# Kernel tuning notes

Hardware: AMD Instinct MI355X
Metric: run time of the kernel (lower is better)

The kernel has to match this reference:

```python
import jax, jax.numpy as jnp
import numpy as np

DIM = 512
HEADS = 8
DIM_HEAD = 64
DIM_INNER = HEADS * DIM_HEAD  # 512
EPS = 1e-12


def setup_inputs() -> dict:
    key = jax.random.key(0)
    ks = jax.random.split(key, 5)
    B, X, Y, N = 8, 32, 32, 1024
    fmap = jax.random.normal(ks[0], (B, DIM, X, Y), dtype=jnp.float32)
    context = jax.random.normal(ks[1], (B, N, DIM), dtype=jnp.float32)
    gamma_fmap = jnp.ones((DIM, 1, 1), dtype=jnp.float32)
    gamma_ctx = jnp.ones((DIM,), dtype=jnp.float32)
    Wq = jax.random.normal(ks[2], (DIM_INNER, DIM), dtype=jnp.float32) * 0.02
    Wkv = jax.random.normal(ks[3], (2 * DIM_INNER, DIM), dtype=jnp.float32) * 0.02
    Wout = jax.random.normal(ks[4], (DIM, DIM_INNER), dtype=jnp.float32) * 0.02
    return {"fmap": fmap, "context": context, "gamma_fmap": gamma_fmap,
            "gamma_ctx": gamma_ctx, "Wq": Wq, "Wkv": Wkv, "Wout": Wout}


def _channel_rmsnorm(x, gamma):
    # F.normalize(x, dim=1) * sqrt(dim) * gamma ; x: [b, c, x, y]
    norm = jnp.sqrt(jnp.sum(x * x, axis=1, keepdims=True))
    normed = x / jnp.maximum(norm, EPS)
    return normed * (DIM ** 0.5) * gamma


def _rmsnorm(x, gamma):
    # F.normalize(x, dim=-1) * sqrt(dim) * gamma ; x: [b, n, d]
    norm = jnp.sqrt(jnp.sum(x * x, axis=-1, keepdims=True))
    normed = x / jnp.maximum(norm, EPS)
    return normed * (DIM ** 0.5) * gamma


def reference(fmap, context, gamma_fmap, gamma_ctx, Wq, Wkv, Wout):
    B, _, X, Y = fmap.shape
    N = context.shape[1]
    H, D = HEADS, DIM_HEAD
    scale = D ** -0.5

    fm = _channel_rmsnorm(fmap, gamma_fmap)          # [b, c, x, y]
    ctx = _rmsnorm(context, gamma_ctx)               # [b, n, c]

    # 1x1 conv == channel matmul
    q = jnp.einsum('bcxy,ec->bexy', fm, Wq)          # [b, h*d, x, y]
    kv = jnp.einsum('bnc,ec->bne', ctx, Wkv)         # [b, n, 2*h*d]
    k, v = jnp.split(kv, 2, axis=-1)

    # q: b (h d) x y -> (b h) (x y) d
    q = q.reshape(B, H, D, X * Y).transpose(0, 1, 3, 2).reshape(B * H, X * Y, D)
    # k, v: b n (h d) -> (b h) n d
    k = k.reshape(B, N, H, D).transpose(0, 2, 1, 3).reshape(B * H, N, D)
    v = v.reshape(B, N, H, D).transpose(0, 2, 1, 3).reshape(B * H, N, D)

    # Euclidean cdist: sqrt(||q||^2 + ||k||^2 - 2 q.k)
    q2 = jnp.sum(q * q, axis=-1)                     # [bh, i]
    k2 = jnp.sum(k * k, axis=-1)                     # [bh, j]
    qk = jnp.einsum('bid,bjd->bij', q, k)            # [bh, i, j]
    dist = jnp.sqrt(jnp.maximum(q2[:, :, None] + k2[:, None, :] - 2.0 * qk, 0.0))
    sim = -dist * scale
    attn = jax.nn.softmax(sim, axis=-1)

    out = jnp.einsum('bij,bjd->bid', attn, v)        # [bh, xy, d]
    # (b h) (x y) d -> b (h d) x y
    out = out.reshape(B, H, X * Y, D).transpose(0, 1, 3, 2).reshape(B, H * D, X, Y)
    return jnp.einsum('bexy,de->bdxy', out, Wout)    # [b, dim, x, y]
```

## Files before the change

### kernel.cpp

```cpp
#include <hip/hip_runtime.h>
#include <math.h>

#define BATCH 8
#define CDIM 512
#define XY 1024
#define NCTX 1024
#define HEADS 8
#define DHEAD 64
#define EINNER 512
#define E2 1024

#define SQRT_DIM 22.627416997969522f

typedef short bf16x8 __attribute__((ext_vector_type(8)));
typedef float f32x4 __attribute__((ext_vector_type(4)));
typedef unsigned short ushort4v __attribute__((ext_vector_type(4)));

__device__ __forceinline__ unsigned short f2bf(float x) {
    unsigned int u = __builtin_bit_cast(unsigned int, x);
    return (unsigned short)((u + 0x7fffu + ((u >> 16) & 1u)) >> 16);
}
__device__ __forceinline__ float bf2f(unsigned short h) {
    unsigned int u = ((unsigned int)h) << 16;
    return __builtin_bit_cast(float, u);
}

__global__ __launch_bounds__(256) void k_fmap_scale(const float* __restrict__ fmap,
                                                    float* __restrict__ fscale) {
    int t = blockIdx.x * 256 + threadIdx.x;
    int b = t >> 10;
    const float* p = fmap + (size_t)b * CDIM * XY + (t & 1023);
    float ss = 0.f;
#pragma unroll 8
    for (int c = 0; c < CDIM; ++c) {
        float v = p[(size_t)c * XY];
        ss = fmaf(v, v, ss);
    }
    fscale[t] = SQRT_DIM / fmaxf(sqrtf(ss), 1e-12f);
}

__global__ __launch_bounds__(256) void k_ctx_scale(const float* __restrict__ ctx,
                                                   float* __restrict__ cscale) {
    int row = blockIdx.x * 4 + (threadIdx.x >> 6);
    int lane = threadIdx.x & 63;
    const float* p = ctx + (size_t)row * CDIM;
    float ss = 0.f;
#pragma unroll
    for (int k = 0; k < CDIM / 64; ++k) {
        float v = p[lane + 64 * k];
        ss = fmaf(v, v, ss);
    }
#pragma unroll
    for (int off = 32; off; off >>= 1) ss += __shfl_down(ss, off, 64);
    if (lane == 0) cscale[row] = SQRT_DIM / fmaxf(sqrtf(ss), 1e-12f);
}

template <bool SCALE_B>
__global__ __launch_bounds__(256) void k_gemm_nn(const float* __restrict__ A,
                                                 const float* __restrict__ Bm,
                                                 float* __restrict__ Cm,
                                                 const float* __restrict__ colscale,
                                                 const float* __restrict__ rowgamma,
                                                 int M, int N, int K) {
    const int b = blockIdx.z;
    const int n0 = blockIdx.x * 64, m0 = blockIdx.y * 64;
    const float* Bb = Bm + (size_t)b * K * N;
    float* Cb = Cm + (size_t)b * M * N;
    __shared__ float As[16][68];
    __shared__ float Bs[16][68];
    const int t = threadIdx.x;
    const int tr = t >> 4, tc = t & 15;
    const int la_k = t & 15, la_m = t >> 4;
    const int lb_n = t & 63, lb_k = t >> 6;
    float acc[4][4] = {};

    float cs = 1.f;
    if constexpr (SCALE_B) cs = colscale[(size_t)b * N + n0 + lb_n];

    for (int k0 = 0; k0 < K; k0 += 16) {
        __syncthreads();
#pragma unroll
        for (int i = 0; i < 4; ++i) {
            int m = la_m + 16 * i;
            As[la_k][m] = A[(size_t)(m0 + m) * K + k0 + la_k];
        }
#pragma unroll
        for (int i = 0; i < 4; ++i) {
            int kk = lb_k + 4 * i;
            float v = Bb[(size_t)(k0 + kk) * N + n0 + lb_n];
            if constexpr (SCALE_B) v *= cs * rowgamma[k0 + kk];
            Bs[kk][lb_n] = v;
        }
        __syncthreads();
#pragma unroll
        for (int kk = 0; kk < 16; ++kk) {
            const float4 a4 = *(const float4*)(&As[kk][tr * 4]);
            const float4 b4 = *(const float4*)(&Bs[kk][tc * 4]);
            const float ar[4] = {a4.x, a4.y, a4.z, a4.w};
            const float bc[4] = {b4.x, b4.y, b4.z, b4.w};
#pragma unroll
            for (int rr = 0; rr < 4; ++rr)
#pragma unroll
                for (int cc = 0; cc < 4; ++cc)
                    acc[rr][cc] = fmaf(ar[rr], bc[cc], acc[rr][cc]);
        }
    }
#pragma unroll
    for (int rr = 0; rr < 4; ++rr) {
        float4 v = {acc[rr][0], acc[rr][1], acc[rr][2], acc[rr][3]};
        *(float4*)(&Cb[(size_t)(m0 + tr * 4 + rr) * N + n0 + tc * 4]) = v;
    }
}

__global__ __launch_bounds__(256) void k_gemm_kv(const float* __restrict__ Am,
                                                 const float* __restrict__ Bmat,
                                                 const float* __restrict__ rowscale,
                                                 const float* __restrict__ kgamma,
                                                 unsigned short* __restrict__ khi,
                                                 unsigned short* __restrict__ klo,
                                                 unsigned short* __restrict__ vthi,
                                                 unsigned short* __restrict__ vtlo,
                                                 float* __restrict__ k2g) {
    const int b = blockIdx.z;
    const int M = NCTX, K = CDIM;
    const int n0 = blockIdx.x * 64, m0 = blockIdx.y * 64;
    const float* Ab = Am + (size_t)b * M * K;
    __shared__ float As[16][68];
    __shared__ float Bs[16][68];
    const int t = threadIdx.x;
    const int tr = t >> 4, tc = t & 15;
    const int la_k = t & 15, la_m = t >> 4;
    float acc[4][4] = {};

    float rs[4];
#pragma unroll
    for (int i = 0; i < 4; ++i)
        rs[i] = rowscale[(size_t)b * M + m0 + la_m + 16 * i];

    for (int k0 = 0; k0 < K; k0 += 16) {
        __syncthreads();
#pragma unroll
        for (int i = 0; i < 4; ++i) {
            int m = la_m + 16 * i;
            float v = Ab[(size_t)(m0 + m) * K + k0 + la_k];
            v *= rs[i] * kgamma[k0 + la_k];
            As[la_k][m] = v;
        }
#pragma unroll
        for (int i = 0; i < 4; ++i) {
            int n = la_m + 16 * i;
            Bs[la_k][n] = Bmat[(size_t)(n0 + n) * K + k0 + la_k];
        }
        __syncthreads();
#pragma unroll
        for (int kk = 0; kk < 16; ++kk) {
            const float4 a4 = *(const float4*)(&As[kk][tr * 4]);
            const float4 b4 = *(const float4*)(&Bs[kk][tc * 4]);
            const float ar[4] = {a4.x, a4.y, a4.z, a4.w};
            const float bc[4] = {b4.x, b4.y, b4.z, b4.w};
#pragma unroll
            for (int rr = 0; rr < 4; ++rr)
#pragma unroll
                for (int cc = 0; cc < 4; ++cc)
                    acc[rr][cc] = fmaf(ar[rr], bc[cc], acc[rr][cc]);
        }
    }

    const int hh = (n0 >> 6) & 7;
    const int bh_i = b * 8 + hh;
    if (n0 < EINNER) {
#pragma unroll
        for (int rr = 0; rr < 4; ++rr) {
            const int n = m0 + tr * 4 + rr;
            ushort4v h4, l4;
#pragma unroll
            for (int cc = 0; cc < 4; ++cc) {
                unsigned short h = f2bf(acc[rr][cc]);
                h4[cc] = h;
                l4[cc] = f2bf(acc[rr][cc] - bf2f(h));
            }
            *(ushort4v*)(khi + ((size_t)bh_i * NCTX + n) * 64 + tc * 4) = h4;
            *(ushort4v*)(klo + ((size_t)bh_i * NCTX + n) * 64 + tc * 4) = l4;
        }
#pragma unroll
        for (int rr = 0; rr < 4; ++rr) {
            float s = 0.f;
#pragma unroll
            for (int cc = 0; cc < 4; ++cc) s = fmaf(acc[rr][cc], acc[rr][cc], s);
            s += __shfl_xor(s, 1, 64);
            s += __shfl_xor(s, 2, 64);
            s += __shfl_xor(s, 4, 64);
            s += __shfl_xor(s, 8, 64);
            if (tc == 0) k2g[(size_t)bh_i * NCTX + m0 + tr * 4 + rr] = s;
        }
    } else {
#pragma unroll
        for (int cc = 0; cc < 4; ++cc) {
            const int d = tc * 4 + cc;
            ushort4v h4, l4;
#pragma unroll
            for (int rr = 0; rr < 4; ++rr) {
                unsigned short h = f2bf(acc[rr][cc]);
                h4[rr] = h;
                l4[rr] = f2bf(acc[rr][cc] - bf2f(h));
            }
            *(ushort4v*)(vthi + ((size_t)bh_i * 64 + d) * NCTX + m0 + tr * 4) = h4;
            *(ushort4v*)(vtlo + ((size_t)bh_i * 64 + d) * NCTX + m0 + tr * 4) = l4;
        }
    }
}

__global__ __launch_bounds__(256) void k_attn_mfma(
    const float* __restrict__ qbuf, const unsigned short* __restrict__ khi,
    const unsigned short* __restrict__ klo, const unsigned short* __restrict__ vthi,
    const unsigned short* __restrict__ vtlo, const float* __restrict__ k2g,
    float* __restrict__ ao) {
    const int bh = blockIdx.y;
    const int i0 = blockIdx.x * 32;
    const int t = threadIdx.x;
    const int w = t >> 6;
    const int rg = w >> 1;
    const int jh = w & 1;
    const int lane = t & 63;
    const int c = lane & 15, g = lane >> 4;

    __shared__ __align__(16) char pool[18432];
    unsigned short* psth = (unsigned short*)(pool + w * 4608);
    unsigned short* pstl = psth + 16 * 72;
    __shared__ float q2s[32];
    __shared__ float msh[4][16];
    __shared__ float lsh[4][16];

    const float* qb = qbuf + (size_t)bh * 64 * XY;
    const int qrow = i0 + 16 * rg + c;
    float qv[16];
#pragma unroll
    for (int kk = 0; kk < 2; ++kk)
#pragma unroll
        for (int i = 0; i < 8; ++i)
            qv[kk * 8 + i] = qb[(size_t)(32 * kk + 8 * g + i) * XY + qrow];

    float s2 = 0.f;
#pragma unroll
    for (int i = 0; i < 16; ++i) s2 = fmaf(qv[i], qv[i], s2);
    s2 += __shfl_xor(s2, 16, 64);
    s2 += __shfl_xor(s2, 32, 64);
    if (g == 0) q2s[16 * rg + c] = s2;
    __syncthreads();
    float q2r[4];
#pragma unroll
    for (int r = 0; r < 4; ++r) q2r[r] = q2s[16 * rg + 4 * g + r];

    bf16x8 qh[2], ql[2];
#pragma unroll
    for (int kk = 0; kk < 2; ++kk)
#pragma unroll
        for (int i = 0; i < 8; ++i) {
            float x = qv[kk * 8 + i];
            unsigned short h = f2bf(x);
            qh[kk][i] = (short)h;
            ql[kk][i] = (short)f2bf(x - bf2f(h));
        }

    const unsigned short* khb = khi + (size_t)bh * NCTX * 64;
    const unsigned short* klb = klo + (size_t)bh * NCTX * 64;
    const unsigned short* vhb = vthi + (size_t)bh * 64 * NCTX;
    const unsigned short* vlb = vtlo + (size_t)bh * 64 * NCTX;
    const float* k2b = k2g + (size_t)bh * NCTX;

    f32x4 acc_o[4] = {{0.f, 0.f, 0.f, 0.f}, {0.f, 0.f, 0.f, 0.f},
                      {0.f, 0.f, 0.f, 0.f}, {0.f, 0.f, 0.f, 0.f}};
    float m_run[4], l_run[4];
#pragma unroll
    for (int r = 0; r < 4; ++r) { m_run[r] = -1e30f; l_run[r] = 0.f; }

    const int jbeg = jh * 512, jend = jbeg + 512;
    for (int j0 = jbeg; j0 < jend; j0 += 64) {
        float p[4][4];
#pragma unroll
        for (int cc = 0; cc < 4; ++cc) {
            const unsigned short* kr_h = khb + (size_t)(j0 + 16 * cc + c) * 64 + 8 * g;
            const unsigned short* kr_l = klb + (size_t)(j0 + 16 * cc + c) * 64 + 8 * g;
            f32x4 acc = {0.f, 0.f, 0.f, 0.f};
#pragma unroll
            for (int kk = 0; kk < 2; ++kk) {
                bf16x8 kh_ = *(const bf16x8*)(kr_h + 32 * kk);
                bf16x8 kl_ = *(const bf16x8*)(kr_l + 32 * kk);
                acc = __builtin_amdgcn_mfma_f32_16x16x32_bf16(qh[kk], kh_, acc, 0, 0, 0);
                acc = __builtin_amdgcn_mfma_f32_16x16x32_bf16(qh[kk], kl_, acc, 0, 0, 0);
                acc = __builtin_amdgcn_mfma_f32_16x16x32_bf16(ql[kk], kh_, acc, 0, 0, 0);
            }
            float k2v = k2b[j0 + 16 * cc + c];
#pragma unroll
            for (int r = 0; r < 4; ++r) {
                float d2 = q2r[r] + k2v - 2.f * acc[r];
                p[cc][r] = -0.125f * sqrtf(fmaxf(d2, 0.f));
            }
        }
        float alpha[4];
#pragma unroll
        for (int r = 0; r < 4; ++r) {
            float mt = fmaxf(fmaxf(p[0][r], p[1][r]), fmaxf(p[2][r], p[3][r]));
            mt = fmaxf(mt, __shfl_xor(mt, 1, 64));
            mt = fmaxf(mt, __shfl_xor(mt, 2, 64));
            mt = fmaxf(mt, __shfl_xor(mt, 4, 64));
            mt = fmaxf(mt, __shfl_xor(mt, 8, 64));
            float mn = fmaxf(m_run[r], mt);
            alpha[r] = __expf(m_run[r] - mn);
            m_run[r] = mn;
            float sum = 0.f;
#pragma unroll
            for (int cc = 0; cc < 4; ++cc) {
                float e = __expf(p[cc][r] - mn);
                p[cc][r] = e;
                sum += e;
            }
            sum += __shfl_xor(sum, 1, 64);
            sum += __shfl_xor(sum, 2, 64);
            sum += __shfl_xor(sum, 4, 64);
            sum += __shfl_xor(sum, 8, 64);
            l_run[r] = l_run[r] * alpha[r] + sum;
        }
#pragma unroll
        for (int dt = 0; dt < 4; ++dt)
#pragma unroll
            for (int r = 0; r < 4; ++r) acc_o[dt][r] *= alpha[r];

#pragma unroll
        for (int cc = 0; cc < 4; ++cc)
#pragma unroll
            for (int r = 0; r < 4; ++r) {
                float x = p[cc][r];
                unsigned short h = f2bf(x);
                psth[(4 * g + r) * 72 + 16 * cc + c] = h;
                pstl[(4 * g + r) * 72 + 16 * cc + c] = f2bf(x - bf2f(h));
            }
        asm volatile("s_waitcnt lgkmcnt(0)" ::: "memory");
        bf16x8 ph[2], pl[2];
#pragma unroll
        for (int kk = 0; kk < 2; ++kk) {
            ph[kk] = *(const bf16x8*)(psth + c * 72 + 32 * kk + 8 * g);
            pl[kk] = *(const bf16x8*)(pstl + c * 72 + 32 * kk + 8 * g);
        }
#pragma unroll
        for (int dt = 0; dt < 4; ++dt) {
            const unsigned short* vr_h = vhb + (size_t)(16 * dt + c) * NCTX + j0 + 8 * g;
            const unsigned short* vr_l = vlb + (size_t)(16 * dt + c) * NCTX + j0 + 8 * g;
#pragma unroll
            for (int kk = 0; kk < 2; ++kk) {
                bf16x8 vh_ = *(const bf16x8*)(vr_h + 32 * kk);
                bf16x8 vl_ = *(const bf16x8*)(vr_l + 32 * kk);
                acc_o[dt] = __builtin_amdgcn_mfma_f32_16x16x32_bf16(ph[kk], vh_, acc_o[dt], 0, 0, 0);
                acc_o[dt] = __builtin_amdgcn_mfma_f32_16x16x32_bf16(ph[kk], vl_, acc_o[dt], 0, 0, 0);
                acc_o[dt] = __builtin_amdgcn_mfma_f32_16x16x32_bf16(pl[kk], vh_, acc_o[dt], 0, 0, 0);
            }
        }
    }

    __syncthreads();
    float* pf = (float*)pool;
#pragma unroll
    for (int dt = 0; dt < 4; ++dt)
#pragma unroll
        for (int r = 0; r < 4; ++r)
            pf[w * 1056 + (4 * g + r) * 66 + 16 * dt + c] = acc_o[dt][r];
    if (c == 0) {
#pragma unroll
        for (int r = 0; r < 4; ++r) {
            msh[w][4 * g + r] = m_run[r];
            lsh[w][4 * g + r] = l_run[r];
        }
    }
    __syncthreads();

    {
        const int q = t & 31, dblk = t >> 5;
        const int qrg = q >> 4, qr = q & 15;
        const int wA = qrg * 2, wB = wA + 1;
        float m1 = msh[wA][qr], m2 = msh[wB][qr];
        float l1 = lsh[wA][qr], l2 = lsh[wB][qr];
        float M = fmaxf(m1, m2);
        float e1 = __expf(m1 - M), e2 = __expf(m2 - M);
        float inv = 1.f / (e1 * l1 + e2 * l2);
        float w1 = e1 * inv, w2 = e2 * inv;
#pragma unroll
        for (int dd = 0; dd < 8; ++dd) {
            int d = dblk * 8 + dd;
            float o1 = pf[wA * 1056 + qr * 66 + d];
            float o2 = pf[wB * 1056 + qr * 66 + d];
            ao[((size_t)bh * 64 + d) * XY + i0 + q] = w1 * o1 + w2 * o2;
        }
    }
}

extern "C" void kernel_launch(void* const* d_in, const int* in_sizes, int n_in,
                              void* d_out, int out_size, void* d_ws, size_t ws_size,
                              hipStream_t stream) {
    const float* fmap    = (const float*)d_in[0];
    const float* context = (const float*)d_in[1];
    const float* gfm     = (const float*)d_in[2];
    const float* gctx    = (const float*)d_in[3];
    const float* Wq      = (const float*)d_in[4];
    const float* Wkv     = (const float*)d_in[5];
    const float* Wout    = (const float*)d_in[6];
    float* out = (float*)d_out;

    float* ws = (float*)d_ws;
    float* fscale = ws;
    float* cscale = ws + 8192;
    float* qbuf   = ws + 16384;
    float* k2g    = ws + 16384 + 4194304;
    unsigned short* khi  = (unsigned short*)(ws + 16384 + 4194304 + 65536);
    unsigned short* klo  = khi + 4194304;
    unsigned short* vthi = klo + 4194304;
    unsigned short* vtlo = vthi + 4194304;

    k_fmap_scale<<<32, 256, 0, stream>>>(fmap, fscale);
    k_ctx_scale<<<2048, 256, 0, stream>>>(context, cscale);

    k_gemm_nn<true><<<dim3(16, 8, BATCH), 256, 0, stream>>>(
        Wq, fmap, qbuf, fscale, gfm, EINNER, XY, CDIM);

    k_gemm_kv<<<dim3(16, 16, BATCH), 256, 0, stream>>>(
        context, Wkv, cscale, gctx, khi, klo, vthi, vtlo, k2g);

    k_attn_mfma<<<dim3(32, 64), 256, 0, stream>>>(
        qbuf, khi, klo, vthi, vtlo, k2g, qbuf);

    k_gemm_nn<false><<<dim3(16, 8, BATCH), 256, 0, stream>>>(
        Wout, qbuf, out, nullptr, nullptr, CDIM, XY, EINNER);
}
```

Before: 619.0 us.

## Move projection GEMMs to split-bf16 MFMA and restage layouts through workspace

Replaces the three fp32 SIMT projection GEMMs (Q, KV, output) with MFMA kernels that use a hi/lo bf16 split with three products to keep near-fp32 accuracy. A prep kernel transposes fmap into channel-last bf16 hi/lo, and a separate pass pre-splits the weights with gamma folded in. The attention kernel now takes pre-split Q and precomputed q norms, uses exp2 with a folded scale, and writes its output transposed and split for the output GEMM. The output buffer and workspace are reused as scratch across stages, which relies on careful aliasing and stream ordering.

```diff
diff --git a/kernel.cpp b/kernel.cpp
--- a/kernel.cpp
+++ b/kernel.cpp
@@ -1,4 +1,5 @@
 #include <hip/hip_runtime.h>
+#include <hip/hip_bf16.h>
 #include <math.h>
 
 #define BATCH 8
@@ -11,32 +12,54 @@
 #define E2 1024
 
 #define SQRT_DIM 22.627416997969522f
+#define NEG_SL2E -0.18033688011112042f
 
 typedef short bf16x8 __attribute__((ext_vector_type(8)));
 typedef float f32x4 __attribute__((ext_vector_type(4)));
-typedef unsigned short ushort4v __attribute__((ext_vector_type(4)));
-
-__device__ __forceinline__ unsigned short f2bf(float x) {
-    unsigned int u = __builtin_bit_cast(unsigned int, x);
-    return (unsigned short)((u + 0x7fffu + ((u >> 16) & 1u)) >> 16);
-}
-__device__ __forceinline__ float bf2f(unsigned short h) {
+typedef unsigned short u16;
+typedef u16 ushort8v __attribute__((ext_vector_type(8)));
+typedef u16 ushort4v __attribute__((ext_vector_type(4)));
+
+__device__ __forceinline__ u16 f2bf(float x) {
+    return __builtin_bit_cast(u16, __float2bfloat16(x));
+}
+__device__ __forceinline__ float bf2f(u16 h) {
     unsigned int u = ((unsigned int)h) << 16;
     return __builtin_bit_cast(float, u);
 }
 
-__global__ __launch_bounds__(256) void k_fmap_scale(const float* __restrict__ fmap,
-                                                    float* __restrict__ fscale) {
-    int t = blockIdx.x * 256 + threadIdx.x;
-    int b = t >> 10;
-    const float* p = fmap + (size_t)b * CDIM * XY + (t & 1023);
+__global__ __launch_bounds__(256) void k_fmap_prep(const float* __restrict__ fmap,
+                                                   u16* __restrict__ fmTh,
+                                                   u16* __restrict__ fmTl,
+                                                   float* __restrict__ fscale) {
+    const int blk = blockIdx.x, b = blk >> 5, x0 = (blk & 31) * 32;
+    const int xy = threadIdx.x & 31, cg = threadIdx.x >> 5;
+    const float* p = fmap + (size_t)b * CDIM * XY + x0 + xy;
+    u16* ph = fmTh + ((size_t)b * 1024 + x0 + xy) * 512 + cg * 64;
+    u16* pl = fmTl + ((size_t)b * 1024 + x0 + xy) * 512 + cg * 64;
     float ss = 0.f;
-#pragma unroll 8
-    for (int c = 0; c < CDIM; ++c) {
-        float v = p[(size_t)c * XY];
-        ss = fmaf(v, v, ss);
-    }
-    fscale[t] = SQRT_DIM / fmaxf(sqrtf(ss), 1e-12f);
+#pragma unroll
+    for (int ii = 0; ii < 8; ++ii) {
+        ushort8v h8, l8;
+#pragma unroll
+        for (int j = 0; j < 8; ++j) {
+            float v = p[(size_t)(cg * 64 + ii * 8 + j) * XY];
+            ss = fmaf(v, v, ss);
+            u16 hh = f2bf(v);
+            h8[j] = hh;
+            l8[j] = f2bf(v - bf2f(hh));
+        }
+        *(ushort8v*)(ph + ii * 8) = h8;
+        *(ushort8v*)(pl + ii * 8) = l8;
+    }
+    __shared__ float red[8][33];
+    red[cg][xy] = ss;
+    __syncthreads();
+    if (threadIdx.x < 32) {
+        float s = red[0][xy] + red[1][xy] + red[2][xy] + red[3][xy]
+                + red[4][xy] + red[5][xy] + red[6][xy] + red[7][xy];
+        fscale[b * XY + x0 + xy] = SQRT_DIM / fmaxf(sqrtf(s), 1e-12f);
+    }
 }
 
 __global__ __launch_bounds__(256) void k_ctx_scale(const float* __restrict__ ctx,
@@ -55,166 +78,208 @@
     if (lane == 0) cscale[row] = SQRT_DIM / fmaxf(sqrtf(ss), 1e-12f);
 }
 
-template <bool SCALE_B>
-__global__ __launch_bounds__(256) void k_gemm_nn(const float* __restrict__ A,
-                                                 const float* __restrict__ Bm,
-                                                 float* __restrict__ Cm,
-                                                 const float* __restrict__ colscale,
-                                                 const float* __restrict__ rowgamma,
-                                                 int M, int N, int K) {
-    const int b = blockIdx.z;
-    const int n0 = blockIdx.x * 64, m0 = blockIdx.y * 64;
-    const float* Bb = Bm + (size_t)b * K * N;
-    float* Cb = Cm + (size_t)b * M * N;
-    __shared__ float As[16][68];
-    __shared__ float Bs[16][68];
-    const int t = threadIdx.x;
-    const int tr = t >> 4, tc = t & 15;
-    const int la_k = t & 15, la_m = t >> 4;
-    const int lb_n = t & 63, lb_k = t >> 6;
-    float acc[4][4] = {};
-
-    float cs = 1.f;
-    if constexpr (SCALE_B) cs = colscale[(size_t)b * N + n0 + lb_n];
-
-    for (int k0 = 0; k0 < K; k0 += 16) {
-        __syncthreads();
-#pragma unroll
-        for (int i = 0; i < 4; ++i) {
-            int m = la_m + 16 * i;
-            As[la_k][m] = A[(size_t)(m0 + m) * K + k0 + la_k];
-        }
-#pragma unroll
-        for (int i = 0; i < 4; ++i) {
-            int kk = lb_k + 4 * i;
-            float v = Bb[(size_t)(k0 + kk) * N + n0 + lb_n];
-            if constexpr (SCALE_B) v *= cs * rowgamma[k0 + kk];
-            Bs[kk][lb_n] = v;
-        }
-        __syncthreads();
-#pragma unroll
-        for (int kk = 0; kk < 16; ++kk) {
-            const float4 a4 = *(const float4*)(&As[kk][tr * 4]);
-            const float4 b4 = *(const float4*)(&Bs[kk][tc * 4]);
-            const float ar[4] = {a4.x, a4.y, a4.z, a4.w};
-            const float bc[4] = {b4.x, b4.y, b4.z, b4.w};
-#pragma unroll
-            for (int rr = 0; rr < 4; ++rr)
-#pragma unroll
-                for (int cc = 0; cc < 4; ++cc)
-                    acc[rr][cc] = fmaf(ar[rr], bc[cc], acc[rr][cc]);
-        }
-    }
-#pragma unroll
-    for (int rr = 0; rr < 4; ++rr) {
-        float4 v = {acc[rr][0], acc[rr][1], acc[rr][2], acc[rr][3]};
-        *(float4*)(&Cb[(size_t)(m0 + tr * 4 + rr) * N + n0 + tc * 4]) = v;
-    }
-}
-
-__global__ __launch_bounds__(256) void k_gemm_kv(const float* __restrict__ Am,
-                                                 const float* __restrict__ Bmat,
-                                                 const float* __restrict__ rowscale,
-                                                 const float* __restrict__ kgamma,
-                                                 unsigned short* __restrict__ khi,
-                                                 unsigned short* __restrict__ klo,
-                                                 unsigned short* __restrict__ vthi,
-                                                 unsigned short* __restrict__ vtlo,
-                                                 float* __restrict__ k2g) {
-    const int b = blockIdx.z;
-    const int M = NCTX, K = CDIM;
-    const int n0 = blockIdx.x * 64, m0 = blockIdx.y * 64;
-    const float* Ab = Am + (size_t)b * M * K;
-    __shared__ float As[16][68];
-    __shared__ float Bs[16][68];
-    const int t = threadIdx.x;
-    const int tr = t >> 4, tc = t & 15;
-    const int la_k = t & 15, la_m = t >> 4;
-    float acc[4][4] = {};
-
-    float rs[4];
-#pragma unroll
-    for (int i = 0; i < 4; ++i)
-        rs[i] = rowscale[(size_t)b * M + m0 + la_m + 16 * i];
-
-    for (int k0 = 0; k0 < K; k0 += 16) {
-        __syncthreads();
-#pragma unroll
-        for (int i = 0; i < 4; ++i) {
-            int m = la_m + 16 * i;
-            float v = Ab[(size_t)(m0 + m) * K + k0 + la_k];
-            v *= rs[i] * kgamma[k0 + la_k];
-            As[la_k][m] = v;
-        }
-#pragma unroll
-        for (int i = 0; i < 4; ++i) {
-            int n = la_m + 16 * i;
-            Bs[la_k][n] = Bmat[(size_t)(n0 + n) * K + k0 + la_k];
-        }
-        __syncthreads();
-#pragma unroll
-        for (int kk = 0; kk < 16; ++kk) {
-            const float4 a4 = *(const float4*)(&As[kk][tr * 4]);
-            const float4 b4 = *(const float4*)(&Bs[kk][tc * 4]);
-            const float ar[4] = {a4.x, a4.y, a4.z, a4.w};
-            const float bc[4] = {b4.x, b4.y, b4.z, b4.w};
-#pragma unroll
-            for (int rr = 0; rr < 4; ++rr)
-#pragma unroll
-                for (int cc = 0; cc < 4; ++cc)
-                    acc[rr][cc] = fmaf(ar[rr], bc[cc], acc[rr][cc]);
-        }
-    }
-
-    const int hh = (n0 >> 6) & 7;
-    const int bh_i = b * 8 + hh;
-    if (n0 < EINNER) {
-#pragma unroll
-        for (int rr = 0; rr < 4; ++rr) {
-            const int n = m0 + tr * 4 + rr;
-            ushort4v h4, l4;
-#pragma unroll
-            for (int cc = 0; cc < 4; ++cc) {
-                unsigned short h = f2bf(acc[rr][cc]);
-                h4[cc] = h;
-                l4[cc] = f2bf(acc[rr][cc] - bf2f(h));
-            }
-            *(ushort4v*)(khi + ((size_t)bh_i * NCTX + n) * 64 + tc * 4) = h4;
-            *(ushort4v*)(klo + ((size_t)bh_i * NCTX + n) * 64 + tc * 4) = l4;
-        }
-#pragma unroll
-        for (int rr = 0; rr < 4; ++rr) {
-            float s = 0.f;
-#pragma unroll
-            for (int cc = 0; cc < 4; ++cc) s = fmaf(acc[rr][cc], acc[rr][cc], s);
+__global__ __launch_bounds__(256) void k_wsplit(const float* __restrict__ src,
+                                                const float* __restrict__ gamma,
+                                                u16* __restrict__ dh,
+                                                u16* __restrict__ dl, int n8) {
+    int i = blockIdx.x * 256 + threadIdx.x;
+    if (i >= n8) return;
+    size_t base = (size_t)i * 8;
+    int k0 = (int)(base & 511);
+    float4 a = *(const float4*)(src + base);
+    float4 b4 = *(const float4*)(src + base + 4);
+    float v[8] = {a.x, a.y, a.z, a.w, b4.x, b4.y, b4.z, b4.w};
+    if (gamma) {
+        float4 g0 = *(const float4*)(gamma + k0);
+        float4 g1 = *(const float4*)(gamma + k0 + 4);
+        v[0] *= g0.x; v[1] *= g0.y; v[2] *= g0.z; v[3] *= g0.w;
+        v[4] *= g1.x; v[5] *= g1.y; v[6] *= g1.z; v[7] *= g1.w;
+    }
+    ushort8v h8, l8;
+#pragma unroll
+    for (int j = 0; j < 8; ++j) {
+        u16 hh = f2bf(v[j]);
+        h8[j] = hh;
+        l8[j] = f2bf(v[j] - bf2f(hh));
+    }
+    *(ushort8v*)(dh + base) = h8;
+    *(ushort8v*)(dl + base) = l8;
+}
+
+__global__ __launch_bounds__(256, 4) void k_gemm_q(
+    const u16* __restrict__ fmTh, const u16* __restrict__ fmTl,
+    const u16* __restrict__ wqh, const u16* __restrict__ wql,
+    const float* __restrict__ fscale,
+    u16* __restrict__ qh_, u16* __restrict__ ql_, float* __restrict__ q2g) {
+    const int b = blockIdx.z, h = blockIdx.y, xy0 = blockIdx.x * 64;
+    const int t = threadIdx.x, w = t >> 6, lane = t & 63;
+    const int c = lane & 15, g = lane >> 4;
+    const u16* Ah = fmTh + ((size_t)b * 1024 + xy0 + 16 * w + c) * 512 + 8 * g;
+    const u16* Al = fmTl + ((size_t)b * 1024 + xy0 + 16 * w + c) * 512 + 8 * g;
+    const u16* Bh0 = wqh + ((size_t)(h * 64) + c) * 512 + 8 * g;
+    const u16* Bl0 = wql + ((size_t)(h * 64) + c) * 512 + 8 * g;
+    f32x4 acc[4] = {{0.f,0.f,0.f,0.f},{0.f,0.f,0.f,0.f},{0.f,0.f,0.f,0.f},{0.f,0.f,0.f,0.f}};
+#pragma unroll 2
+    for (int k0 = 0; k0 < 512; k0 += 32) {
+        bf16x8 ah = *(const bf16x8*)(Ah + k0);
+        bf16x8 al = *(const bf16x8*)(Al + k0);
+#pragma unroll
+        for (int ct = 0; ct < 4; ++ct) {
+            bf16x8 bh_ = *(const bf16x8*)(Bh0 + (size_t)ct * 16 * 512 + k0);
+            bf16x8 bl_ = *(const bf16x8*)(Bl0 + (size_t)ct * 16 * 512 + k0);
+            acc[ct] = __builtin_amdgcn_mfma_f32_16x16x32_bf16(ah, bh_, acc[ct], 0, 0, 0);
+            acc[ct] = __builtin_amdgcn_mfma_f32_16x16x32_bf16(ah, bl_, acc[ct], 0, 0, 0);
+            acc[ct] = __builtin_amdgcn_mfma_f32_16x16x32_bf16(al, bh_, acc[ct], 0, 0, 0);
+        }
+    }
+    const int bh = b * 8 + h;
+    const float4 fs4 = *(const float4*)(fscale + b * 1024 + xy0 + 16 * w + 4 * g);
+    const float fsr[4] = {fs4.x, fs4.y, fs4.z, fs4.w};
+    float s2[4] = {0.f, 0.f, 0.f, 0.f};
+#pragma unroll
+    for (int ct = 0; ct < 4; ++ct)
+#pragma unroll
+        for (int r = 0; r < 4; ++r) {
+            float v = acc[ct][r] * fsr[r];
+            u16 hh = f2bf(v);
+            size_t adr = ((size_t)bh * 1024 + xy0 + 16 * w + 4 * g + r) * 64 + 16 * ct + c;
+            qh_[adr] = hh;
+            ql_[adr] = f2bf(v - bf2f(hh));
+            s2[r] = fmaf(v, v, s2[r]);
+        }
+#pragma unroll
+    for (int r = 0; r < 4; ++r) {
+        float s = s2[r];
+        s += __shfl_xor(s, 1, 64);
+        s += __shfl_xor(s, 2, 64);
+        s += __shfl_xor(s, 4, 64);
+        s += __shfl_xor(s, 8, 64);
+        if (c == 0) q2g[(size_t)bh * 1024 + xy0 + 16 * w + 4 * g + r] = s;
+    }
+}
+
+__global__ __launch_bounds__(256, 4) void k_gemm_kv(
+    const float* __restrict__ ctx, const u16* __restrict__ wkvh,
+    const u16* __restrict__ wkvl, const float* __restrict__ cscale,
+    u16* __restrict__ khi, u16* __restrict__ klo,
+    u16* __restrict__ vthi, u16* __restrict__ vtlo, float* __restrict__ k2g) {
+    const int b = blockIdx.z, et = blockIdx.y, n0 = blockIdx.x * 64;
+    const int t = threadIdx.x, w = t >> 6, lane = t & 63;
+    const int c = lane & 15, g = lane >> 4;
+    __shared__ u16 vl[4][2][64][24];
+    const float* Ap = ctx + ((size_t)b * 1024 + n0 + 16 * w + c) * 512 + 8 * g;
+    const u16* Bh0 = wkvh + ((size_t)(et * 64) + c) * 512 + 8 * g;
+    const u16* Bl0 = wkvl + ((size_t)(et * 64) + c) * 512 + 8 * g;
+    f32x4 acc[4] = {{0.f,0.f,0.f,0.f},{0.f,0.f,0.f,0.f},{0.f,0.f,0.f,0.f},{0.f,0.f,0.f,0.f}};
+#pragma unroll 2
+    for (int k0 = 0; k0 < 512; k0 += 32) {
+        float4 a0 = *(const float4*)(Ap + k0);
+        float4 a1 = *(const float4*)(Ap + k0 + 4);
+        float av[8] = {a0.x, a0.y, a0.z, a0.w, a1.x, a1.y, a1.z, a1.w};
+        bf16x8 ah, al;
+#pragma unroll
+        for (int j = 0; j < 8; ++j) {
+            u16 hh = f2bf(av[j]);
+            ah[j] = (short)hh;
+            al[j] = (short)f2bf(av[j] - bf2f(hh));
+        }
+#pragma unroll
+        for (int ct = 0; ct < 4; ++ct) {
+            bf16x8 bh_ = *(const bf16x8*)(Bh0 + (size_t)ct * 16 * 512 + k0);
+            bf16x8 bl_ = *(const bf16x8*)(Bl0 + (size_t)ct * 16 * 512 + k0);
+            acc[ct] = __builtin_amdgcn_mfma_f32_16x16x32_bf16(ah, bh_, acc[ct], 0, 0, 0);
+            acc[ct] = __builtin_amdgcn_mfma_f32_16x16x32_bf16(ah, bl_, acc[ct], 0, 0, 0);
+            acc[ct] = __builtin_amdgcn_mfma_f32_16x16x32_bf16(al, bh_, acc[ct], 0, 0, 0);
+        }
+    }
+    const float4 cs4 = *(const float4*)(cscale + b * 1024 + n0 + 16 * w + 4 * g);
+    const float csr[4] = {cs4.x, cs4.y, cs4.z, cs4.w};
+    if (et < 8) {
+        const int bh = b * 8 + et;
+        float s2[4] = {0.f, 0.f, 0.f, 0.f};
+#pragma unroll
+        for (int ct = 0; ct < 4; ++ct)
+#pragma unroll
+            for (int r = 0; r < 4; ++r) {
+                float v = acc[ct][r] * csr[r];
+                u16 hh = f2bf(v);
+                size_t adr = ((size_t)bh * 1024 + n0 + 16 * w + 4 * g + r) * 64 + 16 * ct + c;
+                khi[adr] = hh;
+                klo[adr] = f2bf(v - bf2f(hh));
+                s2[r] = fmaf(v, v, s2[r]);
+            }
+#pragma unroll
+        for (int r = 0; r < 4; ++r) {
+            float s = s2[r];
             s += __shfl_xor(s, 1, 64);
             s += __shfl_xor(s, 2, 64);
             s += __shfl_xor(s, 4, 64);
             s += __shfl_xor(s, 8, 64);
-            if (tc == 0) k2g[(size_t)bh_i * NCTX + m0 + tr * 4 + rr] = s;
+            if (c == 0) k2g[(size_t)bh * 1024 + n0 + 16 * w + 4 * g + r] = s;
         }
     } else {
-#pragma unroll
-        for (int cc = 0; cc < 4; ++cc) {
-            const int d = tc * 4 + cc;
-            ushort4v h4, l4;
-#pragma unroll
-            for (int rr = 0; rr < 4; ++rr) {
-                unsigned short h = f2bf(acc[rr][cc]);
-                h4[rr] = h;
-                l4[rr] = f2bf(acc[rr][cc] - bf2f(h));
-            }
-            *(ushort4v*)(vthi + ((size_t)bh_i * 64 + d) * NCTX + m0 + tr * 4) = h4;
-            *(ushort4v*)(vtlo + ((size_t)bh_i * 64 + d) * NCTX + m0 + tr * 4) = l4;
-        }
-    }
-}
-
-__global__ __launch_bounds__(256) void k_attn_mfma(
-    const float* __restrict__ qbuf, const unsigned short* __restrict__ khi,
-    const unsigned short* __restrict__ klo, const unsigned short* __restrict__ vthi,
-    const unsigned short* __restrict__ vtlo, const float* __restrict__ k2g,
-    float* __restrict__ ao) {
+        const int h = et - 8, bh = b * 8 + h;
+#pragma unroll
+        for (int ct = 0; ct < 4; ++ct)
+#pragma unroll
+            for (int r = 0; r < 4; ++r) {
+                float v = acc[ct][r] * csr[r];
+                u16 hh = f2bf(v);
+                vl[w][0][16 * ct + c][4 * g + r] = hh;
+                vl[w][1][16 * ct + c][4 * g + r] = f2bf(v - bf2f(hh));
+            }
+        const int d = lane;
+        ushort8v h0 = *(const ushort8v*)(&vl[w][0][d][0]);
+        ushort8v h1 = *(const ushort8v*)(&vl[w][0][d][8]);
+        ushort8v l0 = *(const ushort8v*)(&vl[w][1][d][0]);
+        ushort8v l1 = *(const ushort8v*)(&vl[w][1][d][8]);
+        size_t base = ((size_t)bh * 64 + d) * 1024 + n0 + 16 * w;
+        *(ushort8v*)(vthi + base) = h0;
+        *(ushort8v*)(vthi + base + 8) = h1;
+        *(ushort8v*)(vtlo + base) = l0;
+        *(ushort8v*)(vtlo + base + 8) = l1;
+    }
+}
+
+__global__ __launch_bounds__(256, 4) void k_gemm_out(
+    const u16* __restrict__ wouth, const u16* __restrict__ woutl,
+    const u16* __restrict__ aoTh, const u16* __restrict__ aoTl,
+    float* __restrict__ out) {
+    const int b = blockIdx.z, m0 = blockIdx.y * 64, n0 = blockIdx.x * 64;
+    const int t = threadIdx.x, w = t >> 6, lane = t & 63;
+    const int c = lane & 15, g = lane >> 4;
+    const u16* Ah = wouth + ((size_t)(m0 + 16 * w) + c) * 512 + 8 * g;
+    const u16* Al = woutl + ((size_t)(m0 + 16 * w) + c) * 512 + 8 * g;
+    const u16* Bh0 = aoTh + ((size_t)b * 1024 + n0 + c) * 512 + 8 * g;
+    const u16* Bl0 = aoTl + ((size_t)b * 1024 + n0 + c) * 512 + 8 * g;
+    f32x4 acc[4] = {{0.f,0.f,0.f,0.f},{0.f,0.f,0.f,0.f},{0.f,0.f,0.f,0.f},{0.f,0.f,0.f,0.f}};
+#pragma unroll 2
+    for (int k0 = 0; k0 < 512; k0 += 32) {
+        bf16x8 ah = *(const bf16x8*)(Ah + k0);
+        bf16x8 al = *(const bf16x8*)(Al + k0);
+#pragma unroll
+        for (int ct = 0; ct < 4; ++ct) {
+            bf16x8 bh_ = *(const bf16x8*)(Bh0 + (size_t)ct * 16 * 512 + k0);
+            bf16x8 bl_ = *(const bf16x8*)(Bl0 + (size_t)ct * 16 * 512 + k0);
+            acc[ct] = __builtin_amdgcn_mfma_f32_16x16x32_bf16(ah, bh_, acc[ct], 0, 0, 0);
+            acc[ct] = __builtin_amdgcn_mfma_f32_16x16x32_bf16(ah, bl_, acc[ct], 0, 0, 0);
+            acc[ct] = __builtin_amdgcn_mfma_f32_16x16x32_bf16(al, bh_, acc[ct], 0, 0, 0);
+        }
+    }
+#pragma unroll
+    for (int ct = 0; ct < 4; ++ct)
+#pragma unroll
+        for (int r = 0; r < 4; ++r)
+            out[((size_t)b * 512 + m0 + 16 * w + 4 * g + r) * 1024 + n0 + 16 * ct + c] =
+                acc[ct][r];
+}
+
+__global__ __launch_bounds__(256, 6) void k_attn_mfma(
+    const u16* __restrict__ q_h, const u16* __restrict__ q_l,
+    const u16* __restrict__ khi, const u16* __restrict__ klo,
+    const u16* __restrict__ vthi, const u16* __restrict__ vtlo,
+    const float* __restrict__ q2g, const float* __restrict__ k2g,
+    u16* __restrict__ aoTh, u16* __restrict__ aoTl) {
     const int bh = blockIdx.y;
     const int i0 = blockIdx.x * 32;
     const int t = threadIdx.x;
@@ -224,172 +289,149 @@
     const int lane = t & 63;
     const int c = lane & 15, g = lane >> 4;
 
-    __shared__ __align__(16) char pool[18432];
-    unsigned short* psth = (unsigned short*)(pool + w * 4608);
-    unsigned short* pstl = psth + 16 * 72;
-    __shared__ float q2s[32];
+    __shared__ __align__(16) char pool[4 * 4864];
+    u16* psth = (u16*)(pool + w * 4864);
+    u16* pstl = psth + 16 * 76;
     __shared__ float msh[4][16];
     __shared__ float lsh[4][16];
 
-    const float* qb = qbuf + (size_t)bh * 64 * XY;
     const int qrow = i0 + 16 * rg + c;
-    float qv[16];
-#pragma unroll
-    for (int kk = 0; kk < 2; ++kk)
-#pragma unroll
-        for (int i = 0; i < 8; ++i)
-            qv[kk * 8 + i] = qb[(size_t)(32 * kk + 8 * g + i) * XY + qrow];
-
-    float s2 = 0.f;
-#pragma unroll
-    for (int i = 0; i < 16; ++i) s2 = fmaf(qv[i], qv[i], s2);
-    s2 += __shfl_xor(s2, 16, 64);
-    s2 += __shfl_xor(s2, 32, 64);
-    if (g == 0) q2s[16 * rg + c] = s2;
-    __syncthreads();
-    float q2r[4];
-#pragma unroll
-    for (int r = 0; r < 4; ++r) q2r[r] = q2s[16 * rg + 4 * g + r];
-
+    const u16* qhp = q_h + ((size_t)bh * 1024 + qrow) * 64 + 8 * g;
+    const u16* qlp = q_l + ((size_t)bh * 1024 + qrow) * 64 + 8 * g;
     bf16x8 qh[2], ql[2];
-#pragma unroll
-    for (int kk = 0; kk < 2; ++kk)
-#pragma unroll
-        for (int i = 0; i < 8; ++i) {
-            float x = qv[kk * 8 + i];
-            unsigned short h = f2bf(x);
-            qh[kk][i] = (short)h;
-            ql[kk][i] = (short)f2bf(x - bf2f(h));
-        }
-
-    const unsigned short* khb = khi + (size_t)bh * NCTX * 64;
-    const unsigned short* klb = klo + (size_t)bh * NCTX * 64;
-    const unsigned short* vhb = vthi + (size_t)bh * 64 * NCTX;
-    const unsigned short* vlb = vtlo + (size_t)bh * 64 * NCTX;
+    qh[0] = *(const bf16x8*)(qhp);
+    qh[1] = *(const bf16x8*)(qhp + 32);
+    ql[0] = *(const bf16x8*)(qlp);
+    ql[1] = *(const bf16x8*)(qlp + 32);
+    const float q2c = q2g[(size_t)bh * 1024 + qrow];
+
+    const u16* khb = khi + (size_t)bh * NCTX * 64;
+    const u16* klb = klo + (size_t)bh * NCTX * 64;
+    const u16* vhb = vthi + (size_t)bh * 64 * NCTX;
+    const u16* vlb = vtlo + (size_t)bh * 64 * NCTX;
     const float* k2b = k2g + (size_t)bh * NCTX;
 
-    f32x4 acc_o[4] = {{0.f, 0.f, 0.f, 0.f}, {0.f, 0.f, 0.f, 0.f},
-                      {0.f, 0.f, 0.f, 0.f}, {0.f, 0.f, 0.f, 0.f}};
-    float m_run[4], l_run[4];
-#pragma unroll
-    for (int r = 0; r < 4; ++r) { m_run[r] = -1e30f; l_run[r] = 0.f; }
+    f32x4 acc_o[4] = {{0.f,0.f,0.f,0.f},{0.f,0.f,0.f,0.f},{0.f,0.f,0.f,0.f},{0.f,0.f,0.f,0.f}};
+    float m_run = -1e30f, l_run = 0.f;
 
     const int jbeg = jh * 512, jend = jbeg + 512;
     for (int j0 = jbeg; j0 < jend; j0 += 64) {
-        float p[4][4];
-#pragma unroll
-        for (int cc = 0; cc < 4; ++cc) {
-            const unsigned short* kr_h = khb + (size_t)(j0 + 16 * cc + c) * 64 + 8 * g;
-            const unsigned short* kr_l = klb + (size_t)(j0 + 16 * cc + c) * 64 + 8 * g;
+        float s[4][4];
+#pragma unroll
+        for (int mm = 0; mm < 4; ++mm) {
+            const u16* kr_h = khb + (size_t)(j0 + 16 * mm + c) * 64 + 8 * g;
+            const u16* kr_l = klb + (size_t)(j0 + 16 * mm + c) * 64 + 8 * g;
             f32x4 acc = {0.f, 0.f, 0.f, 0.f};
 #pragma unroll
             for (int kk = 0; kk < 2; ++kk) {
                 bf16x8 kh_ = *(const bf16x8*)(kr_h + 32 * kk);
                 bf16x8 kl_ = *(const bf16x8*)(kr_l + 32 * kk);
-                acc = __builtin_amdgcn_mfma_f32_16x16x32_bf16(qh[kk], kh_, acc, 0, 0, 0);
-                acc = __builtin_amdgcn_mfma_f32_16x16x32_bf16(qh[kk], kl_, acc, 0, 0, 0);
-                acc = __builtin_amdgcn_mfma_f32_16x16x32_bf16(ql[kk], kh_, acc, 0, 0, 0);
-            }
-            float k2v = k2b[j0 + 16 * cc + c];
+                acc = __builtin_amdgcn_mfma_f32_16x16x32_bf16(kh_, qh[kk], acc, 0, 0, 0);
+                acc = __builtin_amdgcn_mfma_f32_16x16x32_bf16(kh_, ql[kk], acc, 0, 0, 0);
+                acc = __builtin_amdgcn_mfma_f32_16x16x32_bf16(kl_, qh[kk], acc, 0, 0, 0);
+            }
+            const float4 kv4 = *(const float4*)(k2b + j0 + 16 * mm + 4 * g);
+            const float k2a[4] = {kv4.x, kv4.y, kv4.z, kv4.w};
 #pragma unroll
             for (int r = 0; r < 4; ++r) {
-                float d2 = q2r[r] + k2v - 2.f * acc[r];
-                p[cc][r] = -0.125f * sqrtf(fmaxf(d2, 0.f));
-            }
-        }
-        float alpha[4];
-#pragma unroll
-        for (int r = 0; r < 4; ++r) {
-            float mt = fmaxf(fmaxf(p[0][r], p[1][r]), fmaxf(p[2][r], p[3][r]));
-            mt = fmaxf(mt, __shfl_xor(mt, 1, 64));
-            mt = fmaxf(mt, __shfl_xor(mt, 2, 64));
-            mt = fmaxf(mt, __shfl_xor(mt, 4, 64));
-            mt = fmaxf(mt, __shfl_xor(mt, 8, 64));
-            float mn = fmaxf(m_run[r], mt);
-            alpha[r] = __expf(m_run[r] - mn);
-            m_run[r] = mn;
-            float sum = 0.f;
-#pragma unroll
-            for (int cc = 0; cc < 4; ++cc) {
-                float e = __expf(p[cc][r] - mn);
-                p[cc][r] = e;
+                float d2 = fmaf(-2.f, acc[r], q2c + k2a[r]);
+                s[mm][r] = NEG_SL2E * sqrtf(fmaxf(d2, 0.f));
+            }
+        }
+        float mt = s[0][0];
+#pragma unroll
+        for (int mm = 0; mm < 4; ++mm)
+#pragma unroll
+            for (int r = 0; r < 4; ++r) mt = fmaxf(mt, s[mm][r]);
+        mt = fmaxf(mt, __shfl_xor(mt, 16, 64));
+        mt = fmaxf(mt, __shfl_xor(mt, 32, 64));
+        float mn = fmaxf(m_run, mt);
+        float alpha = exp2f(m_run - mn);
+        m_run = mn;
+        float sum = 0.f;
+#pragma unroll
+        for (int mm = 0; mm < 4; ++mm)
+#pragma unroll
+            for (int r = 0; r < 4; ++r) {
+                float e = exp2f(s[mm][r] - mn);
+                s[mm][r] = e;
                 sum += e;
             }
-            sum += __shfl_xor(sum, 1, 64);
-            sum += __shfl_xor(sum, 2, 64);
-            sum += __shfl_xor(sum, 4, 64);
-            sum += __shfl_xor(sum, 8, 64);
-            l_run[r] = l_run[r] * alpha[r] + sum;
-        }
+        sum += __shfl_xor(sum, 16, 64);
+        sum += __shfl_xor(sum, 32, 64);
+        l_run = l_run * alpha + sum;
 #pragma unroll
         for (int dt = 0; dt < 4; ++dt)
 #pragma unroll
-            for (int r = 0; r < 4; ++r) acc_o[dt][r] *= alpha[r];
-
-#pragma unroll
-        for (int cc = 0; cc < 4; ++cc)
+            for (int r = 0; r < 4; ++r) acc_o[dt][r] *= alpha;
+
+#pragma unroll
+        for (int mm = 0; mm < 4; ++mm) {
+            ushort4v h4, l4;
 #pragma unroll
             for (int r = 0; r < 4; ++r) {
-                float x = p[cc][r];
-                unsigned short h = f2bf(x);
-                psth[(4 * g + r) * 72 + 16 * cc + c] = h;
-                pstl[(4 * g + r) * 72 + 16 * cc + c] = f2bf(x - bf2f(h));
-            }
-        asm volatile("s_waitcnt lgkmcnt(0)" ::: "memory");
+                u16 hh = f2bf(s[mm][r]);
+                h4[r] = hh;
+                l4[r] = f2bf(s[mm][r] - bf2f(hh));
+            }
+            *(ushort4v*)(psth + c * 76 + 16 * mm + 4 * g) = h4;
+            *(ushort4v*)(pstl + c * 76 + 16 * mm + 4 * g) = l4;
+        }
         bf16x8 ph[2], pl[2];
 #pragma unroll
         for (int kk = 0; kk < 2; ++kk) {
-            ph[kk] = *(const bf16x8*)(psth + c * 72 + 32 * kk + 8 * g);
-            pl[kk] = *(const bf16x8*)(pstl + c * 72 + 32 * kk + 8 * g);
+            ph[kk] = *(const bf16x8*)(psth + c * 76 + 32 * kk + 8 * g);
+            pl[kk] = *(const bf16x8*)(pstl + c * 76 + 32 * kk + 8 * g);
         }
 #pragma unroll
         for (int dt = 0; dt < 4; ++dt) {
-            const unsigned short* vr_h = vhb + (size_t)(16 * dt + c) * NCTX + j0 + 8 * g;
-            const unsigned short* vr_l = vlb + (size_t)(16 * dt + c) * NCTX + j0 + 8 * g;
+            const u16* vr_h = vhb + (size_t)(16 * dt + c) * NCTX + j0 + 8 * g;
+            const u16* vr_l = vlb + (size_t)(16 * dt + c) * NCTX + j0 + 8 * g;
 #pragma unroll
             for (int kk = 0; kk < 2; ++kk) {
                 bf16x8 vh_ = *(const bf16x8*)(vr_h + 32 * kk);
                 bf16x8 vl_ = *(const bf16x8*)(vr_l + 32 * kk);
-                acc_o[dt] = __builtin_amdgcn_mfma_f32_16x16x32_bf16(ph[kk], vh_, acc_o[dt], 0, 0, 0);
-                acc_o[dt] = __builtin_amdgcn_mfma_f32_16x16x32_bf16(ph[kk], vl_, acc_o[dt], 0, 0, 0);
-                acc_o[dt] = __builtin_amdgcn_mfma_f32_16x16x32_bf16(pl[kk], vh_, acc_o[dt], 0, 0, 0);
-            }
-        }
-    }
-
+                acc_o[dt] = __builtin_amdgcn_mfma_f32_16x16x32_bf16(vh_, ph[kk], acc_o[dt], 0, 0, 0);
+                acc_o[dt] = __builtin_amdgcn_mfma_f32_16x16x32_bf16(vh_, pl[kk], acc_o[dt], 0, 0, 0);
+                acc_o[dt] = __builtin_amdgcn_mfma_f32_16x16x32_bf16(vl_, ph[kk], acc_o[dt], 0, 0, 0);
+            }
+        }
+    }
+
+    float* pfw = (float*)(pool + w * 4864);
+#pragma unroll
+    for (int dt = 0; dt < 4; ++dt)
+#pragma unroll
+        for (int r = 0; r < 4; ++r)
+            pfw[(16 * dt + 4 * g + r) * 18 + c] = acc_o[dt][r];
+    if (g == 0) { msh[w][c] = m_run; lsh[w][c] = l_run; }
     __syncthreads();
-    float* pf = (float*)pool;
-#pragma unroll
-    for (int dt = 0; dt < 4; ++dt)
-#pragma unroll
-        for (int r = 0; r < 4; ++r)
-            pf[w * 1056 + (4 * g + r) * 66 + 16 * dt + c] = acc_o[dt][r];
-    if (c == 0) {
-#pragma unroll
-        for (int r = 0; r < 4; ++r) {
-            msh[w][4 * g + r] = m_run[r];
-            lsh[w][4 * g + r] = l_run[r];
-        }
-    }
-    __syncthreads();
 
     {
-        const int q = t & 31, dblk = t >> 5;
-        const int qrg = q >> 4, qr = q & 15;
-        const int wA = qrg * 2, wB = wA + 1;
-        float m1 = msh[wA][qr], m2 = msh[wB][qr];
-        float l1 = lsh[wA][qr], l2 = lsh[wB][qr];
-        float M = fmaxf(m1, m2);
-        float e1 = __expf(m1 - M), e2 = __expf(m2 - M);
-        float inv = 1.f / (e1 * l1 + e2 * l2);
-        float w1 = e1 * inv, w2 = e2 * inv;
+        const int cq = t & 15, rgq = (t >> 4) & 1, dblk = t >> 5;
+        const int wA = 2 * rgq, wB = wA + 1;
+        const float m1 = msh[wA][cq], m2 = msh[wB][cq];
+        const float l1 = lsh[wA][cq], l2 = lsh[wB][cq];
+        const float M = fmaxf(m1, m2);
+        const float e1 = exp2f(m1 - M), e2 = exp2f(m2 - M);
+        const float inv = 1.f / (e1 * l1 + e2 * l2);
+        const float w1 = e1 * inv, w2 = e2 * inv;
+        const float* pA = (const float*)(pool + wA * 4864);
+        const float* pB = (const float*)(pool + wB * 4864);
+        const int b = bh >> 3, h = bh & 7;
+        const int xy = i0 + 16 * rgq + cq;
+        ushort8v h8, l8;
 #pragma unroll
         for (int dd = 0; dd < 8; ++dd) {
             int d = dblk * 8 + dd;
-            float o1 = pf[wA * 1056 + qr * 66 + d];
-            float o2 = pf[wB * 1056 + qr * 66 + d];
-            ao[((size_t)bh * 64 + d) * XY + i0 + q] = w1 * o1 + w2 * o2;
-        }
+            float o = w1 * pA[d * 18 + cq] + w2 * pB[d * 18 + cq];
+            u16 hh = f2bf(o);
+            h8[dd] = hh;
+            l8[dd] = f2bf(o - bf2f(hh));
+        }
+        size_t adr = ((size_t)b * 1024 + xy) * 512 + h * 64 + dblk * 8;
+        *(ushort8v*)(aoTh + adr) = h8;
+        *(ushort8v*)(aoTl + adr) = l8;
     }
 }
 
@@ -405,28 +447,47 @@
     const float* Wout    = (const float*)d_in[6];
     float* out = (float*)d_out;
 
-    float* ws = (float*)d_ws;
-    float* fscale = ws;
-    float* cscale = ws + 8192;
-    float* qbuf   = ws + 16384;
-    float* k2g    = ws + 16384 + 4194304;
-    unsigned short* khi  = (unsigned short*)(ws + 16384 + 4194304 + 65536);
-    unsigned short* klo  = khi + 4194304;
-    unsigned short* vthi = klo + 4194304;
-    unsigned short* vtlo = vthi + 4194304;
-
-    k_fmap_scale<<<32, 256, 0, stream>>>(fmap, fscale);
+    char* wsb = (char*)d_ws;
+    u16* fmTh = (u16*)(wsb);
+    u16* fmTl = (u16*)(wsb + (8u << 20));
+    u16* khi  = fmTh;
+    u16* klo  = fmTl;
+    u16* vthi = (u16*)(wsb + (16u << 20));
+    u16* vtlo = (u16*)(wsb + (24u << 20));
+    u16* q_h  = (u16*)(wsb + (32u << 20));
+    u16* q_l  = (u16*)(wsb + (40u << 20));
+    u16* aoTh = (u16*)(wsb + (48u << 20));
+    u16* aoTl = (u16*)(wsb + (56u << 20));
+    u16* wouth = (u16*)(wsb);
+    u16* woutl = (u16*)(wsb + 524288 * 2);
+
+    u16* du = (u16*)d_out;
+    u16* wkvh = du;
+    u16* wkvl = du + 524288;
+    u16* wqh  = du + 1048576;
+    u16* wql  = du + 1310720;
+    float* df = (float*)((char*)d_out + (4u << 20));
+    float* q2g    = df;
+    float* k2g    = df + 65536;
+    float* fscale = df + 131072;
+    float* cscale = df + 139264;
+
+    k_fmap_prep<<<256, 256, 0, stream>>>(fmap, fmTh, fmTl, fscale);
     k_ctx_scale<<<2048, 256, 0, stream>>>(context, cscale);
-
-    k_gemm_nn<true><<<dim3(16, 8, BATCH), 256, 0, stream>>>(
-        Wq, fmap, qbuf, fscale, gfm, EINNER, XY, CDIM);
+    k_wsplit<<<128, 256, 0, stream>>>(Wq, gfm, wqh, wql, 512 * 512 / 8);
+    k_wsplit<<<256, 256, 0, stream>>>(Wkv, gctx, wkvh, wkvl, 1024 * 512 / 8);
+
+    k_gemm_q<<<dim3(16, 8, BATCH), 256, 0, stream>>>(
+        fmTh, fmTl, wqh, wql, fscale, q_h, q_l, q2g);
 
     k_gemm_kv<<<dim3(16, 16, BATCH), 256, 0, stream>>>(
-        context, Wkv, cscale, gctx, khi, klo, vthi, vtlo, k2g);
+        context, wkvh, wkvl, cscale, khi, klo, vthi, vtlo, k2g);
 
     k_attn_mfma<<<dim3(32, 64), 256, 0, stream>>>(
-        qbuf, khi, klo, vthi, vtlo, k2g, qbuf);
-
-    k_gemm_nn<false><<<dim3(16, 8, BATCH), 256, 0, stream>>>(
-        Wout, qbuf, out, nullptr, nullptr, CDIM, XY, EINNER);
-}
+        q_h, q_l, khi, klo, vthi, vtlo, q2g, k2g, aoTh, aoTl);
+
+    k_wsplit<<<128, 256, 0, stream>>>(Wout, nullptr, wouth, woutl, 512 * 512 / 8);
+
+    k_gemm_out<<<dim3(16, 8, BATCH), 256, 0, stream>>>(
+        wouth, woutl, aoTh, aoTl, out);
+}
```

Result: slower. 740.4 us (+19.6%).
